# Optimization experiments

Measured on AMD Instinct MI355X. Metric: run time of the kernel, lower is better.

Reference implementation:

```python
import jax, jax.numpy as jnp
import numpy as np

N_NODES = 50000
N_EDGES = 800000
N_FEAT = 128
N_HID = 256
N_PAIRS = 100000


def _gcn_norm(edge_index, n_nodes):
    # add self loops, compute D^-1/2 (A+I) D^-1/2 edge weights (PyG gcn_norm)
    loops = jnp.arange(n_nodes, dtype=edge_index.dtype)
    row = jnp.concatenate([edge_index[0], loops])
    col = jnp.concatenate([edge_index[1], loops])
    deg = jax.ops.segment_sum(jnp.ones_like(col, dtype=jnp.float32), col,
                              num_segments=n_nodes)
    dinv = jnp.where(deg > 0, jax.lax.rsqrt(deg), 0.0)
    norm = dinv[row] * dinv[col]  # [E + N]
    return row, col, norm


def _gcn_conv(x, W, b, row, col, norm, n_nodes):
    h = x @ W                       # [N, out]
    msg = h[row] * norm[:, None]    # gather + scale  [E+N, out]
    agg = jax.ops.segment_sum(msg, col, num_segments=n_nodes)  # scatter-add
    return agg + b


def setup_inputs() -> dict:
    key = jax.random.key(0)
    ks = jax.random.split(key, 9)
    edge_index = jax.random.randint(ks[0], (2, N_EDGES), 0, N_NODES, dtype=jnp.int64)
    features = jax.random.normal(ks[1], (N_NODES, N_FEAT), dtype=jnp.float32)
    mask = jax.random.randint(ks[2], (N_PAIRS, 2), 0, N_NODES, dtype=jnp.int64)
    s1 = 1.0 / np.sqrt(N_FEAT)
    s2 = 1.0 / np.sqrt(N_HID)
    W1 = jax.random.uniform(ks[3], (N_FEAT, N_HID), jnp.float32, -s1, s1)
    b1 = jnp.zeros((N_HID,), jnp.float32)
    W2 = jax.random.uniform(ks[4], (N_HID, N_FEAT), jnp.float32, -s2, s2)
    b2 = jnp.zeros((N_FEAT,), jnp.float32)
    Wl = jax.random.uniform(ks[5], (N_HID, 1), jnp.float32, -s2, s2)
    bl = jax.random.uniform(ks[6], (1,), jnp.float32, -s2, s2)
    return {"edge_index": edge_index, "features": features, "mask": mask,
            "W1": W1, "b1": b1, "W2": W2, "b2": b2, "Wl": Wl, "bl": bl}


def reference(edge_index, features, mask, W1, b1, W2, b2, Wl, bl):
    n = features.shape[0]
    row, col, norm = _gcn_norm(edge_index, n)
    h = _gcn_conv(features, W1, b1, row, col, norm, n)   # GCNConv a
    h = jax.nn.relu(h)                                   # dropout p=0 -> identity
    h = _gcn_conv(h, W2, b2, row, col, norm, n)          # GCNConv b
    mt = mask.T
    p1 = jax.lax.stop_gradient(h[mt[0]])                 # .detach()
    p2 = jax.lax.stop_gradient(h[mt[1]])
    hp = jnp.concatenate([p1, p2], axis=1)               # [n_pairs, 2*n_feat]
    return jax.nn.sigmoid(hp @ Wl + bl)
```

## Files before the change

kernel.cpp:

```cpp
#include <hip/hip_runtime.h>
#include <math.h>

#define NFEAT 128
#define NHID 256
#define NBLK 128

typedef __attribute__((ext_vector_type(8))) short short8;
typedef __attribute__((ext_vector_type(4))) float f32x4;

__device__ inline unsigned short f2bf(float f) {
  unsigned u = __float_as_uint(f);
  u += 0x7fffu + ((u >> 16) & 1u);
  return (unsigned short)(u >> 16);
}
__device__ inline float bflo(unsigned u) { return __uint_as_float(u << 16); }
__device__ inline float bfhi(unsigned u) { return __uint_as_float(u & 0xffff0000u); }


__device__ inline void packOne(const float* __restrict__ W,
                               unsigned short* __restrict__ Wp, int idx, int KS,
                               int OUT) {
  int lane = idx & 63;
  int t = idx >> 6;
  int ks = t % KS;
  int nt = t / KS;
  int n = nt * 16 + (lane & 15);
  int k0 = ks * 32 + (lane >> 4) * 8;
  unsigned short v[8];
#pragma unroll
  for (int j = 0; j < 8; j++) v[j] = f2bf(W[(size_t)(k0 + j) * OUT + n]);
  *reinterpret_cast<short8*>(Wp + (size_t)idx * 8) =
      *reinterpret_cast<short8*>(v);
}

__global__ __launch_bounds__(1024) void k_hist_pack(
    const int* __restrict__ col, int* __restrict__ hist2d, int nE, int nb,
    const float* __restrict__ W1, const float* __restrict__ W2,
    unsigned short* __restrict__ W1p, unsigned short* __restrict__ W2p) {
  if (blockIdx.x >= NBLK) {
    int idx = (blockIdx.x - NBLK) * 1024 + threadIdx.x;
    if (idx < 4096) packOne(W1, W1p, idx, 4, 256);
    else packOne(W2, W2p, idx - 4096, 8, 128);
    return;
  }
  __shared__ int h[1024];
  for (int i = threadIdx.x; i < nb; i += 1024) h[i] = 0;
  __syncthreads();
  int chunk = (nE + NBLK - 1) / NBLK;
  int beg = blockIdx.x * chunk, end = min(beg + chunk, nE);
  for (int e = beg + threadIdx.x; e < end; e += 1024)
    atomicAdd(&h[col[e] >> 6], 1);
  __syncthreads();
  for (int i = threadIdx.x; i < nb; i += 1024)
    hist2d[i * NBLK + blockIdx.x] = h[i];
}

__global__ __launch_bounds__(256) void k_bsum(const int* __restrict__ a,
                                              int* __restrict__ psum, int S,
                                              const float* __restrict__ b2,
                                              const float* __restrict__ Wl,
                                              const float* __restrict__ bl,
                                              float* __restrict__ Cbuf) {
  int t = threadIdx.x;
  if (blockIdx.x == gridDim.x - 1) {
    float v = (t < 128) ? b2[t] * (Wl[t] + Wl[128 + t]) : 0.f;
#pragma unroll
    for (int o = 32; o; o >>= 1) v += __shfl_down(v, o);
    __shared__ float fw[4];
    if ((t & 63) == 0) fw[t >> 6] = v;
    __syncthreads();
    if (t == 0) Cbuf[0] = fw[0] + fw[1] + fw[2] + fw[3] + bl[0];
    return;
  }
  int i = blockIdx.x * 256 + t;
  int v = (i < S) ? a[i] : 0;
#pragma unroll
  for (int o = 32; o; o >>= 1) v += __shfl_down(v, o);
  __shared__ int ws[4];
  if ((t & 63) == 0) ws[t >> 6] = v;
  __syncthreads();
  if (t == 0) psum[blockIdx.x] = ws[0] + ws[1] + ws[2] + ws[3];
}

__global__ __launch_bounds__(256) void k_s3m(const int* __restrict__ a,
                                             const int* __restrict__ psum,
                                             int* __restrict__ out, int S) {
  __shared__ int sh[256];
  __shared__ int ws[4];
  int t = threadIdx.x;
  int b = blockIdx.x;
  int partial = 0;
  for (int i = t; i < b; i += 256) partial += psum[i];
#pragma unroll
  for (int o = 32; o; o >>= 1) partial += __shfl_down(partial, o);
  if ((t & 63) == 0) ws[t >> 6] = partial;
  int i = b * 256 + t;
  int d = (i < S) ? a[i] : 0;
  sh[t] = d;
  __syncthreads();
  int base = ws[0] + ws[1] + ws[2] + ws[3];
  for (int o = 1; o < 256; o <<= 1) {
    int u = (t >= o) ? sh[t - o] : 0;
    __syncthreads();
    sh[t] += u;
    __syncthreads();
  }
  if (i < S) out[i] = base + sh[t] - d;
}

__global__ __launch_bounds__(1024) void k_part2(const int* __restrict__ row,
                                                const int* __restrict__ col,
                                                const int* __restrict__ sbase,
                                                unsigned* __restrict__ tmp,
                                                int nE, int nb) {
  __shared__ int cur[1024];
  for (int i = threadIdx.x; i < nb; i += 1024)
    cur[i] = sbase[i * NBLK + blockIdx.x];
  __syncthreads();
  int chunk = (nE + NBLK - 1) / NBLK;
  int beg = blockIdx.x * chunk, end = min(beg + chunk, nE);
  for (int e = beg + threadIdx.x; e < end; e += 1024) {
    int c = col[e];
    int pos = atomicAdd(&cur[c >> 6], 1);
    tmp[pos] = ((unsigned)(c & 63) << 16) | (unsigned)row[e];
  }
}

__global__ __launch_bounds__(256) void k_bsort_cvt(
    const unsigned* __restrict__ tmp, const int* __restrict__ sbase,
    int* __restrict__ ebuf, int* __restrict__ offs, float* __restrict__ dinv,
    const float* __restrict__ feat, unsigned short* __restrict__ xs, int n,
    int nE, int nb) {
  __shared__ int bins[64], cur[64];
  __shared__ float sdinv[64];
  int b = blockIdx.x;
  int beg = sbase[b * NBLK];
  int end = (b == nb - 1) ? nE : sbase[(b + 1) * NBLK];
  int t = threadIdx.x;
  if (t == 0 && b == nb - 1) offs[n] = nE;
  if (t < 64) bins[t] = 0;
  __syncthreads();
  for (int i = beg + t; i < end; i += 256) atomicAdd(&bins[tmp[i] >> 16], 1);
  __syncthreads();
  if (t < 64) {
    int v = bins[t];
    int s = v;
#pragma unroll
    for (int o = 1; o < 64; o <<= 1) {
      int u = __shfl_up(s, o);
      if (t >= o) s += u;
    }
    int off = beg + s - v;
    cur[t] = off;
    float dv = rsqrtf((float)(v + 1));
    sdinv[t] = dv;
    int node = b * 64 + t;
    if (node < n) {
      offs[node] = off;
      dinv[node] = dv;
    }
  }
  __syncthreads();
  for (int i = beg + t; i < end; i += 256) {
    unsigned p = tmp[i];
    int pos = atomicAdd(&cur[p >> 16], 1);
    ebuf[pos] = (int)(p & 0xffffu);
  }
  for (int i = t; i < 4 * 64 * 8; i += 256) {
    int s = i >> 9;
    int r = (i >> 3) & 63;
    int ch = i & 7;
    int node = b * 64 + r;
    if (node >= n) continue;
    float d = sdinv[r];
    float4 v =
        reinterpret_cast<const float4*>(feat)[(size_t)node * 32 + s * 8 + ch];
    unsigned short o[4] = {f2bf(v.x * d), f2bf(v.y * d), f2bf(v.z * d),
                           f2bf(v.w * d)};
    reinterpret_cast<ushort4*>(xs)[((size_t)s * n + node) * 8 + ch] =
        *reinterpret_cast<ushort4*>(o);
  }
}

__global__ __launch_bounds__(256) void k_agg_bf(
    const unsigned int* __restrict__ G, const int* __restrict__ offs,
    const int* __restrict__ ebuf, const float* __restrict__ dinv,
    unsigned int* __restrict__ OUTP, int n, int nbn, int zs) {
  int slice = blockIdx.x / nbn;
  int node = (blockIdx.x - slice * nbn) * 4 + (threadIdx.x >> 6);
  if (node >= n) return;
  int lane = threadIdx.x & 63;
  int g = lane >> 2;
  int c = lane & 3;
  int beg = offs[node], end = offs[node + 1];
  float acc[8];
  if (g == 0) {
    uint4 s = *reinterpret_cast<const uint4*>(G + ((size_t)slice * n + node) * 16 + c * 4);
    acc[0] = bflo(s.x); acc[1] = bfhi(s.x); acc[2] = bflo(s.y); acc[3] = bfhi(s.y);
    acc[4] = bflo(s.z); acc[5] = bfhi(s.z); acc[6] = bflo(s.w); acc[7] = bfhi(s.w);
  } else {
#pragma unroll
    for (int j = 0; j < 8; j++) acc[j] = 0.f;
  }
  for (int e = beg + g; e < end; e += 16) {
    int src = ebuf[e];
    uint4 v = *reinterpret_cast<const uint4*>(G + ((size_t)slice * n + src) * 16 + c * 4);
    acc[0] += bflo(v.x); acc[1] += bfhi(v.x);
    acc[2] += bflo(v.y); acc[3] += bfhi(v.y);
    acc[4] += bflo(v.z); acc[5] += bfhi(v.z);
    acc[6] += bflo(v.w); acc[7] += bfhi(v.w);
  }
#pragma unroll
  for (int j = 0; j < 8; j++) {
    acc[j] += __shfl_down(acc[j], 32);
    acc[j] += __shfl_down(acc[j], 16);
    acc[j] += __shfl_down(acc[j], 8);
    acc[j] += __shfl_down(acc[j], 4);
  }
  if (g == 0) {
    float d = dinv[node];
    unsigned o[4];
#pragma unroll
    for (int k = 0; k < 4; k++)
      o[k] = (unsigned)f2bf(acc[2 * k] * d) |
             ((unsigned)f2bf(acc[2 * k + 1] * d) << 16);
    *reinterpret_cast<uint4*>(OUTP + ((size_t)slice * zs + node) * 16 + c * 4) =
        *reinterpret_cast<uint4*>(o);
  }
}

__global__ __launch_bounds__(256) void k_mfma_fused(
    const unsigned short* __restrict__ A, const unsigned short* __restrict__ B1p,
    const unsigned short* __restrict__ B2p, const float* __restrict__ b1,
    const float* __restrict__ dinv, const float* __restrict__ Wl,
    float* __restrict__ P, int zs) {
  __shared__ unsigned short sh1[32 * 264];
  __shared__ float pacc[32][2];
  int rt0 = blockIdx.x * 2;
  int wave = threadIdx.x >> 6;
  int lane = threadIdx.x & 63;
  int quad = lane >> 4;
  int mrow0 = rt0 * 16 + (lane & 15);
  if (threadIdx.x < 64) pacc[threadIdx.x >> 1][threadIdx.x & 1] = 0.f;

  f32x4 acc[2][4] = {};
#pragma unroll
  for (int ks = 0; ks < 4; ks++) {
    short8 a0 = *reinterpret_cast<const short8*>(
        A + ((size_t)ks * zs + mrow0) * 32 + quad * 8);
    short8 a1 = *reinterpret_cast<const short8*>(
        A + ((size_t)ks * zs + mrow0 + 16) * 32 + quad * 8);
#pragma unroll
    for (int ct = 0; ct < 4; ct++) {
      int nt = wave * 4 + ct;
      short8 b = *reinterpret_cast<const short8*>(
          B1p + ((size_t)(nt * 4 + ks) * 64 + lane) * 8);
      acc[0][ct] = __builtin_amdgcn_mfma_f32_16x16x32_bf16(a0, b, acc[0][ct], 0, 0, 0);
      acc[1][ct] = __builtin_amdgcn_mfma_f32_16x16x32_bf16(a1, b, acc[1][ct], 0, 0, 0);
    }
  }
#pragma unroll
  for (int ct = 0; ct < 4; ct++) {
    int c = (wave * 4 + ct) * 16 + (lane & 15);
    float bv = b1[c];
#pragma unroll
    for (int rg = 0; rg < 2; rg++)
#pragma unroll
      for (int i = 0; i < 4; i++) {
        float v = fmaxf(acc[rg][ct][i] + bv, 0.f);
        sh1[(rg * 16 + quad * 4 + i) * 264 + c] = f2bf(v);
      }
  }
  __syncthreads();

  f32x4 acc2[2][2] = {};
  const unsigned short* a2_0 = sh1 + (size_t)(lane & 15) * 264 + quad * 8;
  const unsigned short* a2_1 = sh1 + (size_t)(16 + (lane & 15)) * 264 + quad * 8;
#pragma unroll
  for (int ks = 0; ks < 8; ks++) {
    short8 a0 = *reinterpret_cast<const short8*>(a2_0 + ks * 32);
    short8 a1 = *reinterpret_cast<const short8*>(a2_1 + ks * 32);
#pragma unroll
    for (int ct = 0; ct < 2; ct++) {
      int nt = wave * 2 + ct;
      short8 b = *reinterpret_cast<const short8*>(
          B2p + ((size_t)(nt * 8 + ks) * 64 + lane) * 8);
      acc2[0][ct] = __builtin_amdgcn_mfma_f32_16x16x32_bf16(a0, b, acc2[0][ct], 0, 0, 0);
      acc2[1][ct] = __builtin_amdgcn_mfma_f32_16x16x32_bf16(a1, b, acc2[1][ct], 0, 0, 0);
    }
  }
  float p1[2][4] = {}, p2[2][4] = {};
#pragma unroll
  for (int rg = 0; rg < 2; rg++) {
    int r0 = (rt0 + rg) * 16 + quad * 4;
    float dv[4];
#pragma unroll
    for (int i = 0; i < 4; i++) dv[i] = dinv[r0 + i];
#pragma unroll
    for (int ct = 0; ct < 2; ct++) {
      int c = (wave * 2 + ct) * 16 + (lane & 15);
      float wl1 = Wl[c], wl2 = Wl[128 + c];
#pragma unroll
      for (int i = 0; i < 4; i++) {
        float v = acc2[rg][ct][i] * dv[i];
        p1[rg][i] = fmaf(v, wl1, p1[rg][i]);
        p2[rg][i] = fmaf(v, wl2, p2[rg][i]);
      }
    }
  }
#pragma unroll
  for (int rg = 0; rg < 2; rg++)
#pragma unroll
    for (int i = 0; i < 4; i++) {
#pragma unroll
      for (int o = 8; o; o >>= 1) {
        p1[rg][i] += __shfl_xor(p1[rg][i], o);
        p2[rg][i] += __shfl_xor(p2[rg][i], o);
      }
    }
  if ((lane & 15) == 0) {
#pragma unroll
    for (int rg = 0; rg < 2; rg++)
#pragma unroll
      for (int i = 0; i < 4; i++) {
        int row = rg * 16 + quad * 4 + i;
        atomicAdd(&pacc[row][0], p1[rg][i]);
        atomicAdd(&pacc[row][1], p2[rg][i]);
      }
  }
  __syncthreads();
  if (threadIdx.x < 64) {
    int row = threadIdx.x >> 1, comp = threadIdx.x & 1;
    P[(size_t)(rt0 * 16 + row) * 2 + comp] = pacc[row][comp];
  }
}

__global__ __launch_bounds__(256) void k_agg_s(const float2* __restrict__ p,
                                               const int* __restrict__ offs,
                                               const int* __restrict__ ebuf,
                                               const float* __restrict__ dinv,
                                               float2* __restrict__ q, int n) {
  int i = blockIdx.x * 64 + (threadIdx.x >> 2);
  if (i >= n) return;
  int sub = threadIdx.x & 3;
  int beg = offs[i], end = offs[i + 1];
  float sx = 0.f, sy = 0.f;
  for (int e = beg + sub; e < end; e += 4) {
    float2 v = p[ebuf[e]];
    sx += v.x;
    sy += v.y;
  }
  sx += __shfl_down(sx, 2);
  sy += __shfl_down(sy, 2);
  sx += __shfl_down(sx, 1);
  sy += __shfl_down(sy, 1);
  if (sub == 0) {
    float2 self = p[i];
    float d = dinv[i];
    q[i] = make_float2((sx + self.x) * d, (sy + self.y) * d);
  }
}

__global__ __launch_bounds__(256) void k_head2(const float2* __restrict__ q,
                                               const int* __restrict__ mask,
                                               const float* __restrict__ Cbuf,
                                               float* __restrict__ out, int P) {
  int p = blockIdx.x * 256 + threadIdx.x;
  if (p >= P) return;
  int m0 = mask[2 * p], m1 = mask[2 * p + 1];
  float s = q[m0].x + q[m1].y + Cbuf[0];
  out[p] = 1.0f / (1.0f + expf(-s));
}

extern "C" void kernel_launch(void* const* d_in, const int* in_sizes, int n_in,
                              void* d_out, int out_size, void* d_ws,
                              size_t ws_size, hipStream_t stream) {
  const int* edge = (const int*)d_in[0];
  const float* feat = (const float*)d_in[1];
  const int* mask = (const int*)d_in[2];
  const float* W1 = (const float*)d_in[3];
  const float* b1 = (const float*)d_in[4];
  const float* W2 = (const float*)d_in[5];
  const float* b2 = (const float*)d_in[6];
  const float* Wl = (const float*)d_in[7];
  const float* bl = (const float*)d_in[8];
  float* out = (float*)d_out;

  const int E = in_sizes[0] / 2;
  const int N = in_sizes[1] / NFEAT;
  const int P = in_sizes[2] / 2;
  const int* rowp = edge;
  const int* colp = edge + E;
  const int nrt = N / 16;
  const int nb = (N + 63) / 64;
  const int S = nb * NBLK;
  const int nS = (S + 255) / 256;
  const int nbn = (N + 3) / 4;
  const int ZS = N + 16;

  auto aln = [](size_t x) { return (x + 255) & ~(size_t)255; };
  char* w = (char*)d_ws;
  int* hist2d = (int*)w;           w += aln((size_t)S * 4);
  int* sbase = (int*)w;            w += aln((size_t)S * 4);
  int* psum = (int*)w;             w += aln((size_t)1024 * 4);
  float* Cbuf = (float*)w;         w += aln(256);
  int* offs = (int*)w;             w += aln((size_t)(N + 1) * 4);
  int* ebuf = (int*)w;             w += aln((size_t)E * 4);
  unsigned* tmp = (unsigned*)w;    w += aln((size_t)E * 4);
  float* dinv = (float*)w;         w += aln((size_t)N * 4 + 1024);
  unsigned short* xs = (unsigned short*)w;  w += aln((size_t)N * NFEAT * 2);
  unsigned short* z = (unsigned short*)w;   w += aln((size_t)4 * ZS * 32 * 2);
  float* p = (float*)w;            w += aln((size_t)(N + 32) * 8);
  float2* q = (float2*)w;          w += aln((size_t)N * 8);
  unsigned short* W1p = (unsigned short*)w; w += aln((size_t)NFEAT * NHID * 2);
  unsigned short* W2p = (unsigned short*)w; w += aln((size_t)NHID * NFEAT * 2);

  k_hist_pack<<<NBLK + 8, 1024, 0, stream>>>(colp, hist2d, E, nb, W1, W2, W1p,
                                             W2p);
  k_bsum<<<nS + 1, 256, 0, stream>>>(hist2d, psum, S, b2, Wl, bl, Cbuf);
  k_s3m<<<nS, 256, 0, stream>>>(hist2d, psum, sbase, S);
  k_part2<<<NBLK, 1024, 0, stream>>>(rowp, colp, sbase, tmp, E, nb);
  k_bsort_cvt<<<nb, 256, 0, stream>>>(tmp, sbase, ebuf, offs, dinv, feat, xs,
                                      N, E, nb);
  k_agg_bf<<<4 * nbn, 256, 0, stream>>>((const unsigned*)xs, offs, ebuf, dinv,
                                        (unsigned*)z, N, nbn, ZS);
  k_mfma_fused<<<(nrt + 1) / 2, 256, 0, stream>>>(z, W1p, W2p, b1, dinv, Wl, p,
                                                  ZS);
  k_agg_s<<<(N + 63) / 64, 256, 0, stream>>>((const float2*)p, offs, ebuf,
                                             dinv, q, N);
  k_head2<<<(P + 255) / 256, 256, 0, stream>>>(q, mask, Cbuf, out, P);
}
```

Measured before the change: 214.2 us.

## Fuse first-layer neighbor aggregation into MFMA kernel via swizzled LDS tile

The separate bf16 aggregation kernel is removed. Its work now runs inside the MFMA kernel: each block gathers neighbor rows for its 32 nodes straight into a swizzled shared-memory tile, then feeds the MFMA A operand from LDS. The features buffer changes from a 4-slice layout to a row-contiguous one, so one 256-byte row is read with 16 lanes per row. This avoids writing and re-reading the intermediate z buffer and saves one launch. The cost is that gather latency now sits inside the MFMA kernel, which has fewer blocks (one per 32 nodes) and less parallelism to hide it.

Result: faster. 180.7 us (-15.6%).

```diff
diff --git a/kernel.cpp b/kernel.cpp
--- a/kernel.cpp
+++ b/kernel.cpp
@@ -7,6 +7,7 @@
 
 typedef __attribute__((ext_vector_type(8))) short short8;
 typedef __attribute__((ext_vector_type(4))) float f32x4;
+typedef __attribute__((ext_vector_type(2))) float f32x2;
 
 __device__ inline unsigned short f2bf(float f) {
   unsigned u = __float_as_uint(f);
@@ -166,90 +167,110 @@
     int pos = atomicAdd(&cur[p >> 16], 1);
     ebuf[pos] = (int)(p & 0xffffu);
   }
-  for (int i = t; i < 4 * 64 * 8; i += 256) {
-    int s = i >> 9;
-    int r = (i >> 3) & 63;
-    int ch = i & 7;
+  for (int i = t; i < 64 * 32; i += 256) {
+    int r = i >> 5;
     int node = b * 64 + r;
-    if (node >= n) continue;
+    if (node >= n) break;
     float d = sdinv[r];
-    float4 v =
-        reinterpret_cast<const float4*>(feat)[(size_t)node * 32 + s * 8 + ch];
+    float4 v = reinterpret_cast<const float4*>(feat)[(size_t)node * 32 + (i & 31)];
     unsigned short o[4] = {f2bf(v.x * d), f2bf(v.y * d), f2bf(v.z * d),
                            f2bf(v.w * d)};
-    reinterpret_cast<ushort4*>(xs)[((size_t)s * n + node) * 8 + ch] =
+    reinterpret_cast<ushort4*>(xs)[(size_t)node * 32 + (i & 31)] =
         *reinterpret_cast<ushort4*>(o);
   }
 }
 
-__global__ __launch_bounds__(256) void k_agg_bf(
-    const unsigned int* __restrict__ G, const int* __restrict__ offs,
+__global__ __launch_bounds__(256) void k_fused(
+    const char* __restrict__ Gb, const int* __restrict__ offs,
     const int* __restrict__ ebuf, const float* __restrict__ dinv,
-    unsigned int* __restrict__ OUTP, int n, int nbn, int zs) {
-  int slice = blockIdx.x / nbn;
-  int node = (blockIdx.x - slice * nbn) * 4 + (threadIdx.x >> 6);
-  if (node >= n) return;
-  int lane = threadIdx.x & 63;
-  int g = lane >> 2;
-  int c = lane & 3;
-  int beg = offs[node], end = offs[node + 1];
-  float acc[8];
-  if (g == 0) {
-    uint4 s = *reinterpret_cast<const uint4*>(G + ((size_t)slice * n + node) * 16 + c * 4);
-    acc[0] = bflo(s.x); acc[1] = bfhi(s.x); acc[2] = bflo(s.y); acc[3] = bfhi(s.y);
-    acc[4] = bflo(s.z); acc[5] = bfhi(s.z); acc[6] = bflo(s.w); acc[7] = bfhi(s.w);
-  } else {
-#pragma unroll
-    for (int j = 0; j < 8; j++) acc[j] = 0.f;
-  }
-  for (int e = beg + g; e < end; e += 16) {
-    int src = ebuf[e];
-    uint4 v = *reinterpret_cast<const uint4*>(G + ((size_t)slice * n + src) * 16 + c * 4);
-    acc[0] += bflo(v.x); acc[1] += bfhi(v.x);
-    acc[2] += bflo(v.y); acc[3] += bfhi(v.y);
-    acc[4] += bflo(v.z); acc[5] += bfhi(v.z);
-    acc[6] += bflo(v.w); acc[7] += bfhi(v.w);
-  }
-#pragma unroll
-  for (int j = 0; j < 8; j++) {
-    acc[j] += __shfl_down(acc[j], 32);
-    acc[j] += __shfl_down(acc[j], 16);
-    acc[j] += __shfl_down(acc[j], 8);
-    acc[j] += __shfl_down(acc[j], 4);
-  }
-  if (g == 0) {
-    float d = dinv[node];
-    unsigned o[4];
-#pragma unroll
-    for (int k = 0; k < 4; k++)
-      o[k] = (unsigned)f2bf(acc[2 * k] * d) |
-             ((unsigned)f2bf(acc[2 * k + 1] * d) << 16);
-    *reinterpret_cast<uint4*>(OUTP + ((size_t)slice * zs + node) * 16 + c * 4) =
-        *reinterpret_cast<uint4*>(o);
-  }
-}
-
-__global__ __launch_bounds__(256) void k_mfma_fused(
-    const unsigned short* __restrict__ A, const unsigned short* __restrict__ B1p,
-    const unsigned short* __restrict__ B2p, const float* __restrict__ b1,
-    const float* __restrict__ dinv, const float* __restrict__ Wl,
-    float* __restrict__ P, int zs) {
-  __shared__ unsigned short sh1[32 * 264];
+    const unsigned short* __restrict__ B1p, const unsigned short* __restrict__ B2p,
+    const float* __restrict__ b1, const float* __restrict__ Wl,
+    float* __restrict__ P, int n) {
+  __shared__ __align__(16) unsigned short sh_z[32 * 128];
+  __shared__ __align__(16) unsigned short sh1[32 * 264];
   __shared__ float pacc[32][2];
   int rt0 = blockIdx.x * 2;
   int wave = threadIdx.x >> 6;
   int lane = threadIdx.x & 63;
   int quad = lane >> 4;
-  int mrow0 = rt0 * 16 + (lane & 15);
   if (threadIdx.x < 64) pacc[threadIdx.x >> 1][threadIdx.x & 1] = 0.f;
 
+  {
+    int g = lane >> 4;
+    int c = lane & 15;
+    unsigned cb = (unsigned)c << 4;
+    int rbase = rt0 * 16;
+    for (int it = 0; it < 8; ++it) {
+      int rin = wave * 8 + it;
+      int node = rbase + rin;
+      f32x2 acc[4] = {};
+      float d = 0.f;
+      if (node < n) {
+        d = dinv[node];
+        int beg = offs[node], end = offs[node + 1];
+        if (g == 0) {
+          uint4 s = *reinterpret_cast<const uint4*>(
+              Gb + (((unsigned)node << 8) | cb));
+          acc[0] = (f32x2){bflo(s.x), bfhi(s.x)};
+          acc[1] = (f32x2){bflo(s.y), bfhi(s.y)};
+          acc[2] = (f32x2){bflo(s.z), bfhi(s.z)};
+          acc[3] = (f32x2){bflo(s.w), bfhi(s.w)};
+        }
+        int e = beg + g;
+        for (; e + 4 < end; e += 8) {
+          int i0 = ebuf[e], i1 = ebuf[e + 4];
+          uint4 v0 = *reinterpret_cast<const uint4*>(
+              Gb + (((unsigned)i0 << 8) | cb));
+          uint4 v1 = *reinterpret_cast<const uint4*>(
+              Gb + (((unsigned)i1 << 8) | cb));
+          acc[0] += (f32x2){bflo(v0.x), bfhi(v0.x)};
+          acc[1] += (f32x2){bflo(v0.y), bfhi(v0.y)};
+          acc[2] += (f32x2){bflo(v0.z), bfhi(v0.z)};
+          acc[3] += (f32x2){bflo(v0.w), bfhi(v0.w)};
+          acc[0] += (f32x2){bflo(v1.x), bfhi(v1.x)};
+          acc[1] += (f32x2){bflo(v1.y), bfhi(v1.y)};
+          acc[2] += (f32x2){bflo(v1.z), bfhi(v1.z)};
+          acc[3] += (f32x2){bflo(v1.w), bfhi(v1.w)};
+        }
+        if (e < end) {
+          uint4 v0 = *reinterpret_cast<const uint4*>(
+              Gb + (((unsigned)ebuf[e] << 8) | cb));
+          acc[0] += (f32x2){bflo(v0.x), bfhi(v0.x)};
+          acc[1] += (f32x2){bflo(v0.y), bfhi(v0.y)};
+          acc[2] += (f32x2){bflo(v0.z), bfhi(v0.z)};
+          acc[3] += (f32x2){bflo(v0.w), bfhi(v0.w)};
+        }
+      }
+#pragma unroll
+      for (int j = 0; j < 4; j++) {
+        acc[j].x += __shfl_down(acc[j].x, 32);
+        acc[j].y += __shfl_down(acc[j].y, 32);
+        acc[j].x += __shfl_down(acc[j].x, 16);
+        acc[j].y += __shfl_down(acc[j].y, 16);
+      }
+      if (g == 0) {
+        unsigned o[4];
+#pragma unroll
+        for (int k = 0; k < 4; k++)
+          o[k] = (unsigned)f2bf(acc[k].x * d) |
+                 ((unsigned)f2bf(acc[k].y * d) << 16);
+        int c_swz = c ^ (rin & 7);
+        *reinterpret_cast<uint4*>(sh_z + rin * 128 + c_swz * 8) =
+            *reinterpret_cast<uint4*>(o);
+      }
+    }
+  }
+  __syncthreads();
+
   f32x4 acc[2][4] = {};
+  int r0a = lane & 15;
+  int xsw = lane & 7;
 #pragma unroll
   for (int ks = 0; ks < 4; ks++) {
-    short8 a0 = *reinterpret_cast<const short8*>(
-        A + ((size_t)ks * zs + mrow0) * 32 + quad * 8);
-    short8 a1 = *reinterpret_cast<const short8*>(
-        A + ((size_t)ks * zs + mrow0 + 16) * 32 + quad * 8);
+    int cA = quad + ks * 4;
+    int cS = (cA ^ xsw) * 8;
+    short8 a0 = *reinterpret_cast<const short8*>(sh_z + r0a * 128 + cS);
+    short8 a1 = *reinterpret_cast<const short8*>(sh_z + (16 + r0a) * 128 + cS);
 #pragma unroll
     for (int ct = 0; ct < 4; ct++) {
       int nt = wave * 4 + ct;
@@ -395,8 +416,6 @@
   const int nb = (N + 63) / 64;
   const int S = nb * NBLK;
   const int nS = (S + 255) / 256;
-  const int nbn = (N + 3) / 4;
-  const int ZS = N + 16;
 
   auto aln = [](size_t x) { return (x + 255) & ~(size_t)255; };
   char* w = (char*)d_ws;
@@ -409,7 +428,6 @@
   unsigned* tmp = (unsigned*)w;    w += aln((size_t)E * 4);
   float* dinv = (float*)w;         w += aln((size_t)N * 4 + 1024);
   unsigned short* xs = (unsigned short*)w;  w += aln((size_t)N * NFEAT * 2);
-  unsigned short* z = (unsigned short*)w;   w += aln((size_t)4 * ZS * 32 * 2);
   float* p = (float*)w;            w += aln((size_t)(N + 32) * 8);
   float2* q = (float2*)w;          w += aln((size_t)N * 8);
   unsigned short* W1p = (unsigned short*)w; w += aln((size_t)NFEAT * NHID * 2);
@@ -422,10 +440,8 @@
   k_part2<<<NBLK, 1024, 0, stream>>>(rowp, colp, sbase, tmp, E, nb);
   k_bsort_cvt<<<nb, 256, 0, stream>>>(tmp, sbase, ebuf, offs, dinv, feat, xs,
                                       N, E, nb);
-  k_agg_bf<<<4 * nbn, 256, 0, stream>>>((const unsigned*)xs, offs, ebuf, dinv,
-                                        (unsigned*)z, N, nbn, ZS);
-  k_mfma_fused<<<(nrt + 1) / 2, 256, 0, stream>>>(z, W1p, W2p, b1, dinv, Wl, p,
-                                                  ZS);
+  k_fused<<<(nrt + 1) / 2, 256, 0, stream>>>((const char*)xs, offs, ebuf, dinv,
+                                             W1p, W2p, b1, Wl, p, N);
   k_agg_s<<<(N + 63) / 64, 256, 0, stream>>>((const float2*)p, offs, ebuf,
                                              dinv, q, N);
   k_head2<<<(P + 255) / 256, 256, 0, stream>>>(q, mask, Cbuf, out, P);
```
